# Kernel optimization log

Measured on AMD Instinct MI355X. Metric: run time of the kernel, lower is better.

The kernel has to match this reference:

```python
import jax, jax.numpy as jnp
import numpy as np
import math

N_NODES = 100000
N_EDGES = 1600000
DIM = 64


def setup_inputs() -> dict:
    key = jax.random.key(0)
    ks = jax.random.split(key, 16)
    s = 1.0 / math.sqrt(DIM)
    inp = {
        "x": jax.random.normal(ks[0], (N_NODES, DIM), jnp.float32),
        "edge_vec": jax.random.normal(ks[1], (N_EDGES, 3), jnp.float32),
        # lin_Q / lin_K / lin_V
        "Wq": jax.random.normal(ks[2], (DIM, DIM), jnp.float32) * s,
        "bq": jnp.zeros((DIM,), jnp.float32),
        "Wk": jax.random.normal(ks[3], (DIM, DIM), jnp.float32) * s,
        "bk": jnp.zeros((DIM,), jnp.float32),
        "Wv": jax.random.normal(ks[4], (DIM, DIM), jnp.float32) * s,
        "bv": jnp.zeros((DIM,), jnp.float32),
        # edge_bias MLP: [4 -> dim -> dim -> 1], SiLU between layers
        "W1": jax.random.normal(ks[5], (4, DIM), jnp.float32) * 0.5,
        "b1": jnp.zeros((DIM,), jnp.float32),
        "W2": jax.random.normal(ks[6], (DIM, DIM), jnp.float32) * s,
        "b2": jnp.zeros((DIM,), jnp.float32),
        "W3": jax.random.normal(ks[7], (DIM, 1), jnp.float32) * s,
        "b3": jnp.zeros((1,), jnp.float32),
        # w_F
        "wF": jax.random.normal(ks[8], (DIM, 1), jnp.float32) * s,
        "bF": jnp.zeros((1,), jnp.float32),
        "edge_index": jax.random.randint(ks[9], (2, N_EDGES), 0, N_NODES, jnp.int32),
    }
    return inp


def reference(x, edge_vec, Wq, bq, Wk, bk, Wv, bv, W1, b1, W2, b2, W3, b3, wF, bF, edge_index):
    n = x.shape[0]
    dim = x.shape[1]
    i = edge_index[0]
    j = edge_index[1]

    # project on nodes (N << E), then gather to edges
    query = (x @ Wq + bq)[j]          # [E, dim]
    key = (x @ Wk + bk)[i]            # [E, dim]
    value = (x @ Wv + bv)[i]          # [E, dim]

    # edge MLP bias on [vec, |vec|]
    edge_len = jnp.linalg.norm(edge_vec, axis=-1, keepdims=True)  # [E, 1]
    edge_attr = jnp.concatenate([edge_vec, edge_len], axis=-1)    # [E, 4]
    h = jax.nn.silu(edge_attr @ W1 + b1)
    h = jax.nn.silu(h @ W2 + b2)
    bias = (h @ W3 + b3)[:, 0]        # [E]

    scores = jnp.sum(query * key, axis=-1) / jnp.sqrt(jnp.asarray(dim, x.dtype)) + bias  # [E]

    # segment softmax over target node j
    smax = jax.ops.segment_max(scores, j, num_segments=n)
    smax = jnp.where(jnp.isfinite(smax), smax, 0.0)
    ex = jnp.exp(scores - smax[j])
    denom = jax.ops.segment_sum(ex, j, num_segments=n)
    alpha = ex / (denom[j] + 1e-16)   # [E]

    # scatter-weighted vector aggregation
    gate = value @ wF + bF            # [E, 1]
    vec_out = jax.ops.segment_sum(alpha[:, None] * gate * edge_vec, j, num_segments=n)  # [N, 3]
    return vec_out
```

## Files before the change

kernel.cpp:

```cpp
#include <hip/hip_runtime.h>
#include <hip/hip_bf16.h>
#include <math.h>

#define DIM 64

typedef __attribute__((ext_vector_type(8))) short bf16x8;
typedef __attribute__((ext_vector_type(4))) float f32x4;
typedef unsigned short ushort_t;

__device__ __forceinline__ float silu_f(float x) {
    float e = __expf(-x);
    return x * __builtin_amdgcn_rcpf(1.0f + e);
}
__device__ __forceinline__ unsigned short f2bf_fast(float x) {
    unsigned u = __builtin_bit_cast(unsigned, x);
    u += 0x7FFFu + ((u >> 16) & 1u);
    return (unsigned short)(u >> 16);
}
__device__ __forceinline__ void wave_sync() {
    __builtin_amdgcn_wave_barrier();
    __builtin_amdgcn_s_waitcnt(0xC07F);
    __builtin_amdgcn_wave_barrier();
}

__global__ __launch_bounds__(64) void k_prep(
    const float* __restrict__ Wv, const float* __restrict__ bv,
    const float* __restrict__ wF, const float* __restrict__ bF,
    float* __restrict__ u, float* __restrict__ c0)
{
    int lane = threadIdx.x;
    float acc = 0.f;
    for (int n = 0; n < 64; ++n) acc += Wv[lane * 64 + n] * wF[n];
    u[lane] = acc;
    float p = bv[lane] * wF[lane];
    #pragma unroll
    for (int off = 32; off; off >>= 1) p += __shfl_xor(p, off, 64);
    if (lane == 0) c0[0] = p + bF[0];
}

__global__ __launch_bounds__(256) void k_proj_mfma(
    const float* __restrict__ x,
    const float* __restrict__ Wq, const float* __restrict__ bq,
    const float* __restrict__ Wk, const float* __restrict__ bk,
    const float* __restrict__ u, const float* __restrict__ c0p,
    ushort_t* __restrict__ Qh, ushort_t* __restrict__ Kh,
    float* __restrict__ gate, int nNodes, int nTiles)
{
    const int tid = threadIdx.x;
    const int lane = tid & 63;
    const int w = tid >> 6;
    const int lanen = lane & 15;
    const int q = lane >> 4;

    bf16x8 Bq[2][4], Bk[2][4];
    #pragma unroll
    for (int c = 0; c < 2; ++c)
        #pragma unroll
        for (int t = 0; t < 4; ++t) {
            bf16x8 vq, vk;
            #pragma unroll
            for (int j = 0; j < 8; ++j) {
                int idx = (c * 32 + q * 8 + j) * 64 + t * 16 + lanen;
                vq[j] = (short)f2bf_fast(Wq[idx]);
                vk[j] = (short)f2bf_fast(Wk[idx]);
            }
            Bq[c][t] = vq; Bk[c][t] = vk;
        }
    float bqv[4], bkv[4];
    #pragma unroll
    for (int t = 0; t < 4; ++t) { bqv[t] = bq[t * 16 + lanen]; bkv[t] = bk[t * 16 + lanen]; }
    float ur0[8], ur1[8];
    #pragma unroll
    for (int j = 0; j < 8; ++j) { ur0[j] = u[q * 8 + j]; ur1[j] = u[32 + q * 8 + j]; }
    const float c0 = c0p[0];

    const int waveId = blockIdx.x * 4 + w;
    const int wstride = gridDim.x * 4;

    for (int tile = waveId; tile < nTiles; tile += wstride) {
        int node0 = tile * 16;
        int nodeA = node0 + lanen;
        int nodeC = (nodeA < nNodes) ? nodeA : (nNodes - 1);
        const float4* xr = (const float4*)(x + (size_t)nodeC * 64);
        float4 xa = xr[q * 2], xb = xr[q * 2 + 1];
        float4 xc = xr[8 + q * 2], xd = xr[8 + q * 2 + 1];

        float g = xa.x * ur0[0] + xa.y * ur0[1] + xa.z * ur0[2] + xa.w * ur0[3]
                + xb.x * ur0[4] + xb.y * ur0[5] + xb.z * ur0[6] + xb.w * ur0[7]
                + xc.x * ur1[0] + xc.y * ur1[1] + xc.z * ur1[2] + xc.w * ur1[3]
                + xd.x * ur1[4] + xd.y * ur1[5] + xd.z * ur1[6] + xd.w * ur1[7];
        g += __shfl_xor(g, 16);
        g += __shfl_xor(g, 32);

        bf16x8 a0, a1;
        a0[0] = (short)f2bf_fast(xa.x); a0[1] = (short)f2bf_fast(xa.y);
        a0[2] = (short)f2bf_fast(xa.z); a0[3] = (short)f2bf_fast(xa.w);
        a0[4] = (short)f2bf_fast(xb.x); a0[5] = (short)f2bf_fast(xb.y);
        a0[6] = (short)f2bf_fast(xb.z); a0[7] = (short)f2bf_fast(xb.w);
        a1[0] = (short)f2bf_fast(xc.x); a1[1] = (short)f2bf_fast(xc.y);
        a1[2] = (short)f2bf_fast(xc.z); a1[3] = (short)f2bf_fast(xc.w);
        a1[4] = (short)f2bf_fast(xd.x); a1[5] = (short)f2bf_fast(xd.y);
        a1[6] = (short)f2bf_fast(xd.z); a1[7] = (short)f2bf_fast(xd.w);

        f32x4 accq[4] = {{0,0,0,0},{0,0,0,0},{0,0,0,0},{0,0,0,0}};
        f32x4 acck[4] = {{0,0,0,0},{0,0,0,0},{0,0,0,0},{0,0,0,0}};
        #pragma unroll
        for (int t = 0; t < 4; ++t) {
            accq[t] = __builtin_amdgcn_mfma_f32_16x16x32_bf16(a0, Bq[0][t], accq[t], 0, 0, 0);
            accq[t] = __builtin_amdgcn_mfma_f32_16x16x32_bf16(a1, Bq[1][t], accq[t], 0, 0, 0);
            acck[t] = __builtin_amdgcn_mfma_f32_16x16x32_bf16(a0, Bk[0][t], acck[t], 0, 0, 0);
            acck[t] = __builtin_amdgcn_mfma_f32_16x16x32_bf16(a1, Bk[1][t], acck[t], 0, 0, 0);
        }

        #pragma unroll
        for (int t = 0; t < 4; ++t)
            #pragma unroll
            for (int r = 0; r < 4; ++r) {
                int node = node0 + q * 4 + r;
                if (node < nNodes) {
                    size_t o = (size_t)node * 64 + t * 16 + lanen;
                    Qh[o] = f2bf_fast(accq[t][r] + bqv[t]);
                    Kh[o] = f2bf_fast(acck[t][r] + bkv[t]);
                }
            }
        if (q == 0 && nodeA < nNodes) gate[nodeA] = g + c0;
    }
}

__global__ __launch_bounds__(256) void k_edge_mfma(
    const int* __restrict__ ei, const int* __restrict__ ej,
    const ushort_t* __restrict__ Qh, const ushort_t* __restrict__ Kh,
    const float* __restrict__ gate, const float* __restrict__ edge_vec,
    const float* __restrict__ W1, const float* __restrict__ b1,
    const float* __restrict__ W2, const float* __restrict__ b2,
    const float* __restrict__ W3, const float* __restrict__ b3,
    float* __restrict__ out4, int nEdges, long nTiles)
{
    __shared__ __align__(16) float4 sW1v[72];
    __shared__ float sB1[64];
    __shared__ float sBias[4][16];
    __shared__ float sDot[4][16];

    const int tid = threadIdx.x;
    const int lane = tid & 63;
    const int w = tid >> 6;
    const int lanen = lane & 15;
    const int q = lane >> 4;

    if (tid < 64) {
        int slot = tid + (tid >> 3);
        sW1v[slot] = make_float4(W1[tid], W1[64 + tid], W1[128 + tid], W1[192 + tid]);
        sB1[tid] = b1[tid];
    }

    bf16x8 Bfrag[2][4];
    #pragma unroll
    for (int c = 0; c < 2; ++c)
        #pragma unroll
        for (int t = 0; t < 4; ++t) {
            bf16x8 v;
            #pragma unroll
            for (int j = 0; j < 8; ++j)
                v[j] = (short)f2bf_fast(W2[(c * 32 + q * 8 + j) * 64 + t * 16 + lanen]);
            Bfrag[c][t] = v;
        }
    float b2r[4], w3r[4];
    #pragma unroll
    for (int t = 0; t < 4; ++t) { b2r[t] = b2[t * 16 + lanen]; w3r[t] = W3[t * 16 + lanen]; }
    const float b3r = b3[0];
    __syncthreads();

    const long wstride = (long)gridDim.x * 4;
    const long t0 = (long)blockIdx.x * 4 + w;

    auto idx_of = [&](long tile, int& ii, int& jj) {
        long es = tile * 16 + lanen;
        long esc = (es < nEdges) ? es : (long)(nEdges - 1);
        ii = ei[esc]; jj = ej[esc];
    };
    auto gather = [&](long tile, int ii, int jj,
                      bf16x8& A, bf16x8& B, bf16x8& C, bf16x8& D, float& G, float4& AT) {
        const bf16x8* qp = (const bf16x8*)(Qh + (size_t)jj * 64);
        A = qp[q]; B = qp[4 + q];
        const bf16x8* kp = (const bf16x8*)(Kh + (size_t)ii * 64);
        C = kp[q]; D = kp[4 + q];
        G = gate[ii];
        long em = tile * 16 + lanen;
        long emc = (em < nEdges) ? em : (long)(nEdges - 1);
        float ax = edge_vec[emc * 3 + 0];
        float ay = edge_vec[emc * 3 + 1];
        float az = edge_vec[emc * 3 + 2];
        AT = make_float4(ax, ay, az, sqrtf(ax * ax + ay * ay + az * az));
    };

    int iC, jC, iN, jN;
    idx_of(t0, iC, jC);
    idx_of(t0 + wstride, iN, jN);
    bf16x8 qa = {}, qb = {}, ka = {}, kb = {};
    float gte = 0.f;
    float4 attr = make_float4(0.f, 0.f, 0.f, 0.f);
    gather(t0, iC, jC, qa, qb, ka, kb, gte, attr);

    for (long tile = t0; tile < nTiles; tile += wstride) {
        int pw0[4], pw1[4];
        #pragma unroll
        for (int jj = 0; jj < 4; ++jj) {
            int d0 = q * 8 + 2 * jj;
            float4 cA = sW1v[d0 + q];
            float4 cB = sW1v[d0 + 1 + q];
            float4 cC = sW1v[d0 + 32 + q + 4];
            float4 cD = sW1v[d0 + 33 + q + 4];
            float p0 = sB1[d0]      + attr.x*cA.x + attr.y*cA.y + attr.z*cA.z + attr.w*cA.w;
            float p1 = sB1[d0 + 1]  + attr.x*cB.x + attr.y*cB.y + attr.z*cB.z + attr.w*cB.w;
            float p2 = sB1[d0 + 32] + attr.x*cC.x + attr.y*cC.y + attr.z*cC.z + attr.w*cC.w;
            float p3 = sB1[d0 + 33] + attr.x*cD.x + attr.y*cD.y + attr.z*cD.z + attr.w*cD.w;
            float h0 = silu_f(p0), h1v = silu_f(p1), h2v = silu_f(p2), h3v = silu_f(p3);
            int r0, r1;
            asm("v_cvt_pk_bf16_f32 %0, %1, %2" : "=v"(r0) : "v"(h0), "v"(h1v));
            asm("v_cvt_pk_bf16_f32 %0, %1, %2" : "=v"(r1) : "v"(h2v), "v"(h3v));
            pw0[jj] = r0; pw1[jj] = r1;
        }
        bf16x8 a0 = __builtin_bit_cast(bf16x8, make_int4(pw0[0], pw0[1], pw0[2], pw0[3]));
        bf16x8 a1 = __builtin_bit_cast(bf16x8, make_int4(pw1[0], pw1[1], pw1[2], pw1[3]));

        f32x4 accd = {0.f, 0.f, 0.f, 0.f};
        accd = __builtin_amdgcn_mfma_f32_16x16x32_bf16(qa, ka, accd, 0, 0, 0);
        accd = __builtin_amdgcn_mfma_f32_16x16x32_bf16(qb, kb, accd, 0, 0, 0);

        f32x4 acc[4] = {{0,0,0,0},{0,0,0,0},{0,0,0,0},{0,0,0,0}};
        #pragma unroll
        for (int t = 0; t < 4; ++t) {
            acc[t] = __builtin_amdgcn_mfma_f32_16x16x32_bf16(a0, Bfrag[0][t], acc[t], 0, 0, 0);
            acc[t] = __builtin_amdgcn_mfma_f32_16x16x32_bf16(a1, Bfrag[1][t], acc[t], 0, 0, 0);
        }

        int iF, jF;
        idx_of(tile + 2 * wstride, iF, jF);
        bf16x8 qa2 = {}, qb2 = {}, ka2 = {}, kb2 = {};
        float gte2 = 0.f;
        float4 attr2 = make_float4(0.f, 0.f, 0.f, 0.f);
        gather(tile + wstride, iN, jN, qa2, qb2, ka2, kb2, gte2, attr2);

        if (q == (lanen >> 2)) {
            int rsel = lanen & 3;
            float d = accd[0];
            d = (rsel == 1) ? accd[1] : d;
            d = (rsel == 2) ? accd[2] : d;
            d = (rsel == 3) ? accd[3] : d;
            sDot[w][lanen] = d;
        }

        float part[4] = {0.f, 0.f, 0.f, 0.f};
        #pragma unroll
        for (int t = 0; t < 4; ++t)
            #pragma unroll
            for (int r = 0; r < 4; ++r)
                part[r] += silu_f(acc[t][r] + b2r[t]) * w3r[t];
        #pragma unroll
        for (int r = 0; r < 4; ++r) {
            part[r] += __shfl_xor(part[r], 1);
            part[r] += __shfl_xor(part[r], 2);
            part[r] += __shfl_xor(part[r], 4);
            part[r] += __shfl_xor(part[r], 8);
        }
        if (lanen == 0)
            *(float4*)&sBias[w][q * 4] = make_float4(part[0], part[1], part[2], part[3]);

        wave_sync();

        float sc = sDot[w][lanen] * 0.125f + sBias[w][lanen] + b3r;
        float ev = __expf(sc);
        long eC = tile * 16 + lanen;
        if (eC < nEdges) {
            float comp = (q == 0) ? attr.x : (q == 1) ? attr.y : attr.z;
            float val = (q == 3) ? ev : ev * gte * comp;
            atomicAdd(out4 + (size_t)jC * 4 + q, val);
        }

        wave_sync();

        iC = iN; jC = jN; iN = iF; jN = jF;
        qa = qa2; qb = qb2; ka = ka2; kb = kb2; gte = gte2; attr = attr2;
    }
}

__global__ __launch_bounds__(256) void k_div(
    const float4* __restrict__ out4, float* __restrict__ out, int nNodes)
{
    int j = blockIdx.x * 256 + threadIdx.x;
    if (j >= nNodes) return;
    float4 v = out4[j];
    float inv = 1.0f / (v.w + 1e-16f);
    out[(size_t)j * 3 + 0] = v.x * inv;
    out[(size_t)j * 3 + 1] = v.y * inv;
    out[(size_t)j * 3 + 2] = v.z * inv;
}

extern "C" void kernel_launch(void* const* d_in, const int* in_sizes, int n_in,
                              void* d_out, int out_size, void* d_ws, size_t ws_size,
                              hipStream_t stream)
{
    const float* x        = (const float*)d_in[0];
    const float* edge_vec = (const float*)d_in[1];
    const float* Wq = (const float*)d_in[2];
    const float* bq = (const float*)d_in[3];
    const float* Wk = (const float*)d_in[4];
    const float* bk = (const float*)d_in[5];
    const float* Wv = (const float*)d_in[6];
    const float* bv = (const float*)d_in[7];
    const float* W1 = (const float*)d_in[8];
    const float* b1 = (const float*)d_in[9];
    const float* W2 = (const float*)d_in[10];
    const float* b2 = (const float*)d_in[11];
    const float* W3 = (const float*)d_in[12];
    const float* b3 = (const float*)d_in[13];
    const float* wF = (const float*)d_in[14];
    const float* bF = (const float*)d_in[15];
    const int*   eidx = (const int*)d_in[16];

    int nNodes = in_sizes[0] / DIM;
    int nEdges = in_sizes[16] / 2;
    const int* ei = eidx;
    const int* ej = eidx + nEdges;

    char* p = (char*)d_ws;
    ushort_t* Qh = (ushort_t*)p;
    ushort_t* Kh = Qh + (size_t)nNodes * DIM;
    p += (size_t)nNodes * DIM * 2 * sizeof(ushort_t);
    float* gate = (float*)p;  p += (size_t)nNodes * sizeof(float);
    float* out4 = (float*)p;  p += (size_t)nNodes * 4 * sizeof(float);
    float* u = (float*)p;     p += 64 * sizeof(float);
    float* c0 = (float*)p;    p += 64 * sizeof(float);

    float* out = (float*)d_out;
    hipMemsetAsync(out4, 0, (size_t)nNodes * 4 * sizeof(float), stream);

    k_prep<<<1, 64, 0, stream>>>(Wv, bv, wF, bF, u, c0);

    int nTilesN = (nNodes + 15) / 16;
    k_proj_mfma<<<512, 256, 0, stream>>>(x, Wq, bq, Wk, bk, u, c0,
                                         Qh, Kh, gate, nNodes, nTilesN);

    long nTilesE = (nEdges + 15) / 16;
    k_edge_mfma<<<2048, 256, 0, stream>>>(ei, ej, Qh, Kh, gate, edge_vec,
                                          W1, b1, W2, b2, W3, b3,
                                          out4, nEdges, nTilesE);

    int nBn = (nNodes + 255) / 256;
    k_div<<<nBn, 256, 0, stream>>>((const float4*)out4, out, nNodes);
}
```

Baseline: 240.7 us.

## Fuse prep and memset into projection kernel, replace LDS score exchange with bpermute

Removes the single-block prep kernel and the memset by having every wave of the projection kernel compute the Wv·wF vector and bias constant itself and zero the output accumulator rows for its nodes. In the edge kernel, the shared-memory exchange of dot products and bias partials, along with its two wave barriers, is replaced by register selects and one ds_bpermute. The projection grid is doubled. This cuts two launches and per-tile synchronisation, at the cost of redundant per-wave prep arithmetic.

```diff
diff --git a/kernel.cpp b/kernel.cpp
--- a/kernel.cpp
+++ b/kernel.cpp
@@ -17,40 +17,37 @@
     u += 0x7FFFu + ((u >> 16) & 1u);
     return (unsigned short)(u >> 16);
 }
-__device__ __forceinline__ void wave_sync() {
-    __builtin_amdgcn_wave_barrier();
-    __builtin_amdgcn_s_waitcnt(0xC07F);
-    __builtin_amdgcn_wave_barrier();
-}
-
-__global__ __launch_bounds__(64) void k_prep(
-    const float* __restrict__ Wv, const float* __restrict__ bv,
-    const float* __restrict__ wF, const float* __restrict__ bF,
-    float* __restrict__ u, float* __restrict__ c0)
-{
-    int lane = threadIdx.x;
-    float acc = 0.f;
-    for (int n = 0; n < 64; ++n) acc += Wv[lane * 64 + n] * wF[n];
-    u[lane] = acc;
-    float p = bv[lane] * wF[lane];
-    #pragma unroll
-    for (int off = 32; off; off >>= 1) p += __shfl_xor(p, off, 64);
-    if (lane == 0) c0[0] = p + bF[0];
-}
 
 __global__ __launch_bounds__(256) void k_proj_mfma(
     const float* __restrict__ x,
     const float* __restrict__ Wq, const float* __restrict__ bq,
     const float* __restrict__ Wk, const float* __restrict__ bk,
-    const float* __restrict__ u, const float* __restrict__ c0p,
+    const float* __restrict__ Wv, const float* __restrict__ bv,
+    const float* __restrict__ wF, const float* __restrict__ bF,
     ushort_t* __restrict__ Qh, ushort_t* __restrict__ Kh,
-    float* __restrict__ gate, int nNodes, int nTiles)
+    float* __restrict__ gate, float* __restrict__ out4,
+    int nNodes, int nTiles)
 {
     const int tid = threadIdx.x;
     const int lane = tid & 63;
     const int w = tid >> 6;
     const int lanen = lane & 15;
     const int q = lane >> 4;
+
+    float accu = 0.f;
+    #pragma unroll
+    for (int n = 0; n < 64; ++n) accu = fmaf(Wv[lane * 64 + n], wF[n], accu);
+    float pc = bv[lane] * wF[lane];
+    #pragma unroll
+    for (int off = 32; off; off >>= 1) pc += __shfl_xor(pc, off, 64);
+    const float c0 = pc + bF[0];
+    const int ubits = __builtin_bit_cast(int, accu);
+    float ur0[8], ur1[8];
+    #pragma unroll
+    for (int j = 0; j < 8; ++j) {
+        ur0[j] = __builtin_bit_cast(float, __builtin_amdgcn_ds_bpermute((q * 8 + j) * 4, ubits));
+        ur1[j] = __builtin_bit_cast(float, __builtin_amdgcn_ds_bpermute((32 + q * 8 + j) * 4, ubits));
+    }
 
     bf16x8 Bq[2][4], Bk[2][4];
     #pragma unroll
@@ -69,10 +66,6 @@
     float bqv[4], bkv[4];
     #pragma unroll
     for (int t = 0; t < 4; ++t) { bqv[t] = bq[t * 16 + lanen]; bkv[t] = bk[t * 16 + lanen]; }
-    float ur0[8], ur1[8];
-    #pragma unroll
-    for (int j = 0; j < 8; ++j) { ur0[j] = u[q * 8 + j]; ur1[j] = u[32 + q * 8 + j]; }
-    const float c0 = c0p[0];
 
     const int waveId = blockIdx.x * 4 + w;
     const int wstride = gridDim.x * 4;
@@ -123,7 +116,10 @@
                     Kh[o] = f2bf_fast(acck[t][r] + bkv[t]);
                 }
             }
-        if (q == 0 && nodeA < nNodes) gate[nodeA] = g + c0;
+        if (nodeA < nNodes) {
+            if (q == 0) gate[nodeA] = g + c0;
+            if (q == 1) *(float4*)(out4 + (size_t)nodeA * 4) = make_float4(0.f, 0.f, 0.f, 0.f);
+        }
     }
 }
 
@@ -138,14 +134,12 @@
 {
     __shared__ __align__(16) float4 sW1v[72];
     __shared__ float sB1[64];
-    __shared__ float sBias[4][16];
-    __shared__ float sDot[4][16];
 
     const int tid = threadIdx.x;
     const int lane = tid & 63;
-    const int w = tid >> 6;
     const int lanen = lane & 15;
     const int q = lane >> 4;
+    const int w = tid >> 6;
 
     if (tid < 64) {
         int slot = tid + (tid >> 3);
@@ -168,6 +162,8 @@
     #pragma unroll
     for (int t = 0; t < 4; ++t) { b2r[t] = b2[t * 16 + lanen]; w3r[t] = W3[t * 16 + lanen]; }
     const float b3r = b3[0];
+    const int rsel = lanen & 3;
+    const int bperm_addr = ((((lanen >> 2) << 4) | lanen) << 2);
     __syncthreads();
 
     const long wstride = (long)gridDim.x * 4;
@@ -241,15 +237,6 @@
         float4 attr2 = make_float4(0.f, 0.f, 0.f, 0.f);
         gather(tile + wstride, iN, jN, qa2, qb2, ka2, kb2, gte2, attr2);
 
-        if (q == (lanen >> 2)) {
-            int rsel = lanen & 3;
-            float d = accd[0];
-            d = (rsel == 1) ? accd[1] : d;
-            d = (rsel == 2) ? accd[2] : d;
-            d = (rsel == 3) ? accd[3] : d;
-            sDot[w][lanen] = d;
-        }
-
         float part[4] = {0.f, 0.f, 0.f, 0.f};
         #pragma unroll
         for (int t = 0; t < 4; ++t)
@@ -263,21 +250,26 @@
             part[r] += __shfl_xor(part[r], 4);
             part[r] += __shfl_xor(part[r], 8);
         }
-        if (lanen == 0)
-            *(float4*)&sBias[w][q * 4] = make_float4(part[0], part[1], part[2], part[3]);
-
-        wave_sync();
-
-        float sc = sDot[w][lanen] * 0.125f + sBias[w][lanen] + b3r;
+
+        float dsel = accd[0];
+        dsel = (rsel == 1) ? accd[1] : dsel;
+        dsel = (rsel == 2) ? accd[2] : dsel;
+        dsel = (rsel == 3) ? accd[3] : dsel;
+        float psel = part[0];
+        psel = (rsel == 1) ? part[1] : psel;
+        psel = (rsel == 2) ? part[2] : psel;
+        psel = (rsel == 3) ? part[3] : psel;
+        float val = fmaf(dsel, 0.125f, psel);
+        int moved = __builtin_amdgcn_ds_bpermute(bperm_addr, __builtin_bit_cast(int, val));
+        float sc = __builtin_bit_cast(float, moved) + b3r;
+
         float ev = __expf(sc);
         long eC = tile * 16 + lanen;
         if (eC < nEdges) {
             float comp = (q == 0) ? attr.x : (q == 1) ? attr.y : attr.z;
-            float val = (q == 3) ? ev : ev * gte * comp;
-            atomicAdd(out4 + (size_t)jC * 4 + q, val);
-        }
-
-        wave_sync();
+            float vout = (q == 3) ? ev : ev * gte * comp;
+            atomicAdd(out4 + (size_t)jC * 4 + q, vout);
+        }
 
         iC = iN; jC = jN; iN = iF; jN = jF;
         qa = qa2; qb = qb2; ka = ka2; kb = kb2; gte = gte2; attr = attr2;
@@ -329,17 +321,12 @@
     p += (size_t)nNodes * DIM * 2 * sizeof(ushort_t);
     float* gate = (float*)p;  p += (size_t)nNodes * sizeof(float);
     float* out4 = (float*)p;  p += (size_t)nNodes * 4 * sizeof(float);
-    float* u = (float*)p;     p += 64 * sizeof(float);
-    float* c0 = (float*)p;    p += 64 * sizeof(float);
 
     float* out = (float*)d_out;
-    hipMemsetAsync(out4, 0, (size_t)nNodes * 4 * sizeof(float), stream);
-
-    k_prep<<<1, 64, 0, stream>>>(Wv, bv, wF, bF, u, c0);
 
     int nTilesN = (nNodes + 15) / 16;
-    k_proj_mfma<<<512, 256, 0, stream>>>(x, Wq, bq, Wk, bk, u, c0,
-                                         Qh, Kh, gate, nNodes, nTilesN);
+    k_proj_mfma<<<1024, 256, 0, stream>>>(x, Wq, bq, Wk, bk, Wv, bv, wF, bF,
+                                          Qh, Kh, gate, out4, nNodes, nTilesN);
 
     long nTilesE = (nEdges + 15) / 16;
     k_edge_mfma<<<2048, 256, 0, stream>>>(ei, ej, Qh, Kh, gate, edge_vec,
```

Measured after the change: 239.9 us. About the same (-0.3%).
